# Kernel tuning notes

Hardware: AMD Instinct MI355X
Metric: run time of the kernel (lower is better)

Reference implementation:

```python
import jax, jax.numpy as jnp
import numpy as np

B, S, DM, H = 4, 2048, 512, 8
HD = DM // H


def setup_inputs() -> dict:
    key = jax.random.key(0)
    ks = jax.random.split(key, 12)
    x = jax.random.normal(ks[0], (B, S, DM), dtype=jnp.float32)
    # causal lower-triangular mask [B, S, S]
    mask = jnp.broadcast_to(jnp.tril(jnp.ones((S, S), dtype=jnp.int32)), (B, S, S))
    # sorted irregular day offsets (trading-day-like), in days
    days_offset = jnp.sort(
        jax.random.uniform(ks[1], (B, S), dtype=jnp.float32) * 3000.0, axis=-1
    )
    scale = 1.0 / np.sqrt(DM)
    Wq = jax.random.normal(ks[2], (DM, DM), dtype=jnp.float32) * scale
    bq = jnp.zeros((DM,), dtype=jnp.float32)
    Wk = jax.random.normal(ks[3], (DM, DM), dtype=jnp.float32) * scale
    bk = jnp.zeros((DM,), dtype=jnp.float32)
    Wv = jax.random.normal(ks[4], (DM, DM), dtype=jnp.float32) * scale
    bv = jnp.zeros((DM,), dtype=jnp.float32)
    Wo = jax.random.normal(ks[5], (DM, DM), dtype=jnp.float32) * scale
    bo = jnp.zeros((DM,), dtype=jnp.float32)
    decay_rate = jnp.float32(0.1)
    return {
        "x": x, "mask": mask, "days_offset": days_offset,
        "Wq": Wq, "bq": bq, "Wk": Wk, "bk": bk,
        "Wv": Wv, "bv": bv, "Wo": Wo, "bo": bo,
        "decay_rate": decay_rate,
    }


def reference(x, mask, days_offset, Wq, bq, Wk, bk, Wv, bv, Wo, bo, decay_rate):
    b, s, _ = x.shape
    # projections (torch Linear: x @ W.T + b), split heads -> [b, h, s, hd]
    def proj(W, bias):
        return (x @ W.T + bias).reshape(b, s, H, HD).transpose(0, 2, 1, 3)
    q, k, v = proj(Wq, bq), proj(Wk, bk), proj(Wv, bv)
    scores = jnp.einsum("bhqd,bhkd->bhqk", q, k) / jnp.sqrt(jnp.float32(HD))
    # temporal decay: exp(-rate * |t_i - t_j|), broadcast over heads
    dist = jnp.abs(days_offset[:, :, None] - days_offset[:, None, :])  # [b,s,s]
    decay = jnp.exp(-decay_rate * dist)
    scores = scores * decay[:, None, :, :]
    scores = jnp.where(mask[:, None, :, :] == 0, -jnp.inf, scores)
    attn = jax.nn.softmax(scores, axis=-1)  # dropout p=0 (eval)
    out = jnp.einsum("bhqk,bhkd->bhqd", attn, v)
    out = out.transpose(0, 2, 1, 3).reshape(b, s, DM)
    return out @ Wo.T + bo
```

## Files before the change

### kernel.cpp

```cpp
#include <hip/hip_runtime.h>
#include <hip/hip_fp16.h>


#define S_LEN 2048
#define DMODEL 512
#define NH 8
#define HD 64

typedef _Float16 half8 __attribute__((ext_vector_type(8)));
typedef _Float16 half4 __attribute__((ext_vector_type(4)));
typedef float floatx4 __attribute__((ext_vector_type(4)));

__device__ __forceinline__ void gload16(const _Float16* g, _Float16* l) {
    __builtin_amdgcn_global_load_lds(
        (const __attribute__((address_space(1))) void*)g,
        (__attribute__((address_space(3))) void*)l, 16, 0, 0);
}

__global__ __launch_bounds__(256) void cast_f32_f16(
    const float* __restrict__ x,
    const float* __restrict__ Wq, const float* __restrict__ Wk,
    const float* __restrict__ Wv, const float* __restrict__ Wo,
    _Float16* __restrict__ xh, _Float16* __restrict__ Wh)
{
    int i = blockIdx.x * 256 + threadIdx.x;
    const float* src; _Float16* dst; int off;
    if (i < 1048576) { src = x; dst = xh; off = i; }
    else {
        int j = i - 1048576;
        int w = j >> 16;
        int within = j & 65535;
        src = (w == 0) ? Wq : (w == 1) ? Wk : (w == 2) ? Wv : Wo;
        dst = Wh + w * (DMODEL * DMODEL);
        off = within;
    }
    float4 v = ((const float4*)src)[off];
    half4 h;
    h.x = (_Float16)v.x; h.y = (_Float16)v.y; h.z = (_Float16)v.z; h.w = (_Float16)v.w;
    *(half4*)(dst + (size_t)off * 4) = h;
}

template <int MODE>
__global__ __launch_bounds__(256) void gemm_k(
    const _Float16* __restrict__ A, const _Float16* __restrict__ Wbase,
    const float* __restrict__ b0, const float* __restrict__ b1,
    const float* __restrict__ b2,
    _Float16* __restrict__ outh, float* __restrict__ outf)
{
    __shared__ _Float16 As[128 * 64];
    __shared__ _Float16 Ws[128 * 64];
    const int t = threadIdx.x;
    const int bm = blockIdx.x, bn = blockIdx.y, z = blockIdx.z;
    const _Float16* Wp = Wbase + (MODE == 0 ? z * (DMODEL * DMODEL) : 0);
    const float* bias = (MODE == 0) ? (z == 0 ? b0 : (z == 1 ? b1 : b2)) : b0;
    const int w = t >> 6, lane = t & 63, l15 = lane & 15, quad = lane >> 4;
    const int wrow = (w >> 1) * 64, wcol = (w & 1) * 64;
    const int lrow = lane >> 3;
    const int sw = (lane & 7) ^ lrow;

    floatx4 acc[4][4] = {};
    for (int kb = 0; kb < 8; ++kb) {
        __syncthreads();
        #pragma unroll
        for (int i = 0; i < 4; ++i) {
            int row0 = w * 32 + i * 8;
            gload16(A  + (size_t)(bm * 128 + row0 + lrow) * DMODEL + kb * 64 + sw * 8, &As[row0 * 64]);
            gload16(Wp + (size_t)(bn * 128 + row0 + lrow) * DMODEL + kb * 64 + sw * 8, &Ws[row0 * 64]);
        }
        __syncthreads();
        #pragma unroll
        for (int kk = 0; kk < 2; ++kk) {
            half8 af[4], bf[4];
            #pragma unroll
            for (int mt = 0; mt < 4; ++mt)
                af[mt] = *(const half8*)(&As[(wrow + mt * 16 + l15) * 64 + (((quad + 4 * kk) ^ (l15 & 7)) * 8)]);
            #pragma unroll
            for (int nt = 0; nt < 4; ++nt)
                bf[nt] = *(const half8*)(&Ws[(wcol + nt * 16 + l15) * 64 + (((quad + 4 * kk) ^ (l15 & 7)) * 8)]);
            #pragma unroll
            for (int mt = 0; mt < 4; ++mt)
                #pragma unroll
                for (int nt = 0; nt < 4; ++nt)
                    acc[mt][nt] = __builtin_amdgcn_mfma_f32_16x16x32_f16(af[mt], bf[nt], acc[mt][nt], 0, 0, 0);
        }
    }
    #pragma unroll
    for (int mt = 0; mt < 4; ++mt)
        #pragma unroll
        for (int nt = 0; nt < 4; ++nt) {
            int n = bn * 128 + wcol + nt * 16 + l15;
            float bvv = bias[n];
            if (MODE == 0 && z == 2) {
                int m0 = bm * 128 + wrow + mt * 16 + quad * 4;
                int b = m0 >> 11, s0 = m0 & 2047;
                int hh = n >> 6, hd = n & 63;
                half4 hv;
                #pragma unroll
                for (int r = 0; r < 4; ++r) hv[r] = (_Float16)(acc[mt][nt][r] + bvv);
                *(half4*)(outh + (size_t)2 * (8192 * 512) +
                          ((size_t)(b * NH + hh) * HD + hd) * S_LEN + s0) = hv;
            } else {
                #pragma unroll
                for (int r = 0; r < 4; ++r) {
                    int m = bm * 128 + wrow + mt * 16 + quad * 4 + r;
                    float val = acc[mt][nt][r] + bvv;
                    if (MODE == 0) {
                        int b = m >> 11, s = m & 2047;
                        int hh = n >> 6, hd = n & 63;
                        outh[(size_t)z * (8192 * 512) +
                             ((size_t)(b * NH + hh) * S_LEN + s) * HD + hd] = (_Float16)val;
                    } else {
                        outf[(size_t)m * DMODEL + n] = val;
                    }
                }
            }
        }
}

__global__ __launch_bounds__(256, 1) void attn_k(
    const _Float16* __restrict__ Qh, const _Float16* __restrict__ Kh,
    const _Float16* __restrict__ Vt, const float* __restrict__ days,
    const float* __restrict__ rate_p, _Float16* __restrict__ Ah)
{
    __shared__ _Float16 Ks[2][64 * 64];
    __shared__ _Float16 Vs[2][64 * 64];
    __shared__ float    eks[2][64];
    __shared__ _Float16 Ps[4][2][16 * 64];

    const int pr = blockIdx.x, h = blockIdx.y, b = blockIdx.z;
    const int t = threadIdx.x, w = t >> 6, lane = t & 63, l15 = lane & 15, quad = lane >> 4;
    const float rate = rate_p[0];
    const size_t bhoff = (size_t)(b * NH + h) * (size_t)(S_LEN * HD);
    const _Float16* Qb = Qh + bhoff;
    const _Float16* Kb = Kh + bhoff;
    const _Float16* Vb = Vt + bhoff;
    const float* daysb = days + b * S_LEN;
    const int lrow = lane >> 3, sw = (lane & 7) ^ lrow;
    const int e7 = l15 & 7;

    auto stage = [&](int kt, int buf) {
        #pragma unroll
        for (int i = 0; i < 2; ++i) {
            int grp = w * 2 + i;
            int row = grp * 8 + lrow;
            gload16(Kb + (size_t)(kt * 64 + row) * HD + sw * 8, &Ks[buf][grp * 512]);
            gload16(Vb + (size_t)row * S_LEN + kt * 64 + sw * 8, &Vs[buf][grp * 512]);
        }
        if (w == 0) {
            float tk0 = daysb[kt * 64];
            float d = daysb[kt * 64 + lane];
            eks[buf][lane] = __expf(fminf(rate * (d - tk0), 80.f));
        }
    };

    auto phase = [&](int qb) {
        const int q0 = qb * 128 + w * 32;
        const int KT = 2 * qb + 1;
        half8 qf[2][2];
        float tq[2]; int qg[2];
        #pragma unroll
        for (int qs = 0; qs < 2; ++qs) {
            qg[qs] = q0 + qs * 16 + l15;
            tq[qs] = daysb[qg[qs]];
            #pragma unroll
            for (int kk = 0; kk < 2; ++kk)
                qf[qs][kk] = *(const half8*)(Qb + (size_t)qg[qs] * HD + kk * 32 + quad * 8);
        }
        floatx4 oacc[2][4] = {};
        float lacc[2] = {0.f, 0.f};

        stage(0, 0);
        for (int kt = 0; kt <= KT; ++kt) {
            __syncthreads();
            if (kt < KT) stage(kt + 1, (kt + 1) & 1);
            const int buf = kt & 1;
            const float tk0 = daysb[kt * 64];
            half8 kf[4][2];
            #pragma unroll
            for (int c = 0; c < 4; ++c)
                #pragma unroll
                for (int kk = 0; kk < 2; ++kk)
                    kf[c][kk] = *(const half8*)(&Ks[buf][(c * 16 + l15) * 64 + (((quad + 4 * kk) ^ e7) * 8)]);
            floatx4 sc[2][4];
            #pragma unroll
            for (int qs = 0; qs < 2; ++qs)
                #pragma unroll
                for (int c = 0; c < 4; ++c) {
                    floatx4 z4 = {};
                    z4 = __builtin_amdgcn_mfma_f32_16x16x32_f16(kf[c][0], qf[qs][0], z4, 0, 0, 0);
                    sc[qs][c] = __builtin_amdgcn_mfma_f32_16x16x32_f16(kf[c][1], qf[qs][1], z4, 0, 0, 0);
                }
            half8 vf[4][2];
            #pragma unroll
            for (int s = 0; s < 4; ++s)
                #pragma unroll
                for (int kk = 0; kk < 2; ++kk)
                    vf[s][kk] = *(const half8*)(&Vs[buf][(s * 16 + l15) * 64 + (((quad + 4 * kk) ^ e7) * 8)]);
            floatx4 ekv[4];
            #pragma unroll
            for (int c = 0; c < 4; ++c)
                ekv[c] = *(const floatx4*)(&eks[buf][c * 16 + quad * 4]);
            float eq[2];
            #pragma unroll
            for (int qs = 0; qs < 2; ++qs)
                eq[qs] = 0.125f * __expf(-rate * (tq[qs] - tk0));
            const bool nm = (kt >= 2 * qb);
            #pragma unroll
            for (int qs = 0; qs < 2; ++qs) {
                #pragma unroll
                for (int c = 0; c < 4; ++c) {
                    float pv[4];
                    #pragma unroll
                    for (int r = 0; r < 4; ++r) {
                        float sv = sc[qs][c][r] * (eq[qs] * ekv[c][r]);
                        float p = __expf(sv - 2.0f);
                        if (nm && (kt * 64 + c * 16 + quad * 4 + r) > qg[qs]) p = 0.f;
                        lacc[qs] += p;
                        pv[r] = p;
                    }
                    half4 hv;
                    hv.x = (_Float16)pv[0]; hv.y = (_Float16)pv[1];
                    hv.z = (_Float16)pv[2]; hv.w = (_Float16)pv[3];
                    *(half4*)(&Ps[w][qs][l15 * 64 + (((2 * c + (quad >> 1)) ^ e7) * 8) + (quad & 1) * 4]) = hv;
                }
            }
            #pragma unroll
            for (int qs = 0; qs < 2; ++qs) {
                half8 pf0 = *(const half8*)(&Ps[w][qs][l15 * 64 + ((quad ^ e7) * 8)]);
                half8 pf1 = *(const half8*)(&Ps[w][qs][l15 * 64 + (((4 + quad) ^ e7) * 8)]);
                #pragma unroll
                for (int s = 0; s < 4; ++s) {
                    oacc[qs][s] = __builtin_amdgcn_mfma_f32_16x16x32_f16(vf[s][0], pf0, oacc[qs][s], 0, 0, 0);
                    oacc[qs][s] = __builtin_amdgcn_mfma_f32_16x16x32_f16(vf[s][1], pf1, oacc[qs][s], 0, 0, 0);
                }
            }
        }

        #pragma unroll
        for (int qs = 0; qs < 2; ++qs) {
            float l = lacc[qs];
            l += __shfl_xor(l, 16);
            l += __shfl_xor(l, 32);
            float linv = 1.0f / l;
            #pragma unroll
            for (int s = 0; s < 4; ++s) {
                half4 hv;
                #pragma unroll
                for (int r = 0; r < 4; ++r) hv[r] = (_Float16)(oacc[qs][s][r] * linv);
                *(half4*)(Ah + ((size_t)(b * S_LEN) + qg[qs]) * DMODEL + h * HD + s * 16 + quad * 4) = hv;
            }
        }
    };

    phase(pr);
    phase(15 - pr);
}

extern "C" void kernel_launch(void* const* d_in, const int* in_sizes, int n_in,
                              void* d_out, int out_size, void* d_ws, size_t ws_size,
                              hipStream_t stream)
{
    const float* x    = (const float*)d_in[0];
    const float* days = (const float*)d_in[2];
    const float* Wq   = (const float*)d_in[3];
    const float* bq   = (const float*)d_in[4];
    const float* Wk   = (const float*)d_in[5];
    const float* bk   = (const float*)d_in[6];
    const float* Wv   = (const float*)d_in[7];
    const float* bv   = (const float*)d_in[8];
    const float* Wo   = (const float*)d_in[9];
    const float* bo   = (const float*)d_in[10];
    const float* rate = (const float*)d_in[11];
    float* out = (float*)d_out;

    _Float16* xh = (_Float16*)d_ws;
    _Float16* Wh = xh + 4194304;
    _Float16* Qh = Wh + 1048576;
    _Float16* Kh = Qh + 4194304;
    _Float16* Vh = Kh + 4194304;
    _Float16* Ah = Vh + 4194304;

    cast_f32_f16<<<5120, 256, 0, stream>>>(x, Wq, Wk, Wv, Wo, xh, Wh);

    dim3 g0(64, 4, 3);
    gemm_k<0><<<g0, 256, 0, stream>>>(xh, Wh, bq, bk, bv, Qh, nullptr);

    dim3 ga(8, NH, 4);
    attn_k<<<ga, 256, 0, stream>>>(Qh, Kh, Vh, days, rate, Ah);

    dim3 g1(64, 4, 1);
    gemm_k<1><<<g1, 256, 0, stream>>>(Ah, Wh + 3 * (DMODEL * DMODEL), bo, bo, bo, nullptr, out);
}
```

Before: 223.4 us.

## Halve attention query tile, double grid, and stage GEMM epilogue through LDS

The attention kernel now gives each wave 16 query rows instead of 32 and pairs 64-row query blocks j and 31-j. This doubles the grid to 512 blocks and lets two blocks share a CU (launch bounds 256,2), which should improve occupancy and balance the causal work. It also prefetches the first K/V tile of the second phase while the first phase finishes. The GEMM epilogue for Q/K and the output projection now goes through an LDS buffer so global stores are 16-byte vectors instead of scattered scalar writes. The cost is less K/V reuse per staged tile and extra LDS traffic in the epilogue.

Result: faster. 206.9 us (-7.4%).

```diff
diff --git a/kernel.cpp b/kernel.cpp
--- a/kernel.cpp
+++ b/kernel.cpp
@@ -49,6 +49,7 @@
 {
     __shared__ _Float16 As[128 * 64];
     __shared__ _Float16 Ws[128 * 64];
+    __shared__ char epbuf[MODE == 0 ? (4 * 16 * 72 * 2) : (4 * 16 * 68 * 4)];
     const int t = threadIdx.x;
     const int bm = blockIdx.x, bn = blockIdx.y, z = blockIdx.z;
     const _Float16* Wp = Wbase + (MODE == 0 ? z * (DMODEL * DMODEL) : 0);
@@ -84,13 +85,14 @@
                     acc[mt][nt] = __builtin_amdgcn_mfma_f32_16x16x32_f16(af[mt], bf[nt], acc[mt][nt], 0, 0, 0);
         }
     }
-    #pragma unroll
-    for (int mt = 0; mt < 4; ++mt)
-        #pragma unroll
-        for (int nt = 0; nt < 4; ++nt) {
-            int n = bn * 128 + wcol + nt * 16 + l15;
-            float bvv = bias[n];
-            if (MODE == 0 && z == 2) {
+
+    if (MODE == 0 && z == 2) {
+        #pragma unroll
+        for (int mt = 0; mt < 4; ++mt)
+            #pragma unroll
+            for (int nt = 0; nt < 4; ++nt) {
+                int n = bn * 128 + wcol + nt * 16 + l15;
+                float bvv = bias[n];
                 int m0 = bm * 128 + wrow + mt * 16 + quad * 4;
                 int b = m0 >> 11, s0 = m0 & 2047;
                 int hh = n >> 6, hd = n & 63;
@@ -99,25 +101,55 @@
                 for (int r = 0; r < 4; ++r) hv[r] = (_Float16)(acc[mt][nt][r] + bvv);
                 *(half4*)(outh + (size_t)2 * (8192 * 512) +
                           ((size_t)(b * NH + hh) * HD + hd) * S_LEN + s0) = hv;
-            } else {
-                #pragma unroll
-                for (int r = 0; r < 4; ++r) {
-                    int m = bm * 128 + wrow + mt * 16 + quad * 4 + r;
-                    float val = acc[mt][nt][r] + bvv;
-                    if (MODE == 0) {
-                        int b = m >> 11, s = m & 2047;
-                        int hh = n >> 6, hd = n & 63;
-                        outh[(size_t)z * (8192 * 512) +
-                             ((size_t)(b * NH + hh) * S_LEN + s) * HD + hd] = (_Float16)val;
-                    } else {
-                        outf[(size_t)m * DMODEL + n] = val;
-                    }
+            }
+    } else {
+        float bv4[4];
+        #pragma unroll
+        for (int nt = 0; nt < 4; ++nt) bv4[nt] = bias[bn * 128 + wcol + nt * 16 + l15];
+        const int rr = lane >> 3, cc = (lane & 7) ^ rr;
+        if (MODE == 0) {
+            _Float16* Ep = (_Float16*)epbuf + w * (16 * 72);
+            const int hq = (bn * 128 + wcol) >> 6;
+            #pragma unroll
+            for (int mt = 0; mt < 4; ++mt) {
+                #pragma unroll
+                for (int nt = 0; nt < 4; ++nt)
+                    #pragma unroll
+                    for (int r = 0; r < 4; ++r)
+                        Ep[(quad * 4 + r) * 72 + nt * 16 + l15] = (_Float16)(acc[mt][nt][r] + bv4[nt]);
+                #pragma unroll
+                for (int i2 = 0; i2 < 2; ++i2) {
+                    int row = i2 * 8 + rr;
+                    half8 v = *(const half8*)(&Ep[row * 72 + cc * 8]);
+                    int m = bm * 128 + wrow + mt * 16 + row;
+                    int bb = m >> 11, ss = m & 2047;
+                    *(half8*)(outh + (size_t)z * (8192 * 512) +
+                              ((size_t)(bb * NH + hq) * S_LEN + ss) * HD + cc * 8) = v;
                 }
             }
-        }
-}
-
-__global__ __launch_bounds__(256, 1) void attn_k(
+        } else {
+            float* Epf = (float*)epbuf + w * (16 * 68);
+            #pragma unroll
+            for (int mt = 0; mt < 4; ++mt) {
+                #pragma unroll
+                for (int nt = 0; nt < 4; ++nt)
+                    #pragma unroll
+                    for (int r = 0; r < 4; ++r)
+                        Epf[(quad * 4 + r) * 68 + nt * 16 + l15] = acc[mt][nt][r] + bv4[nt];
+                #pragma unroll
+                for (int i2 = 0; i2 < 4; ++i2) {
+                    int row = (i2 & 1) * 8 + rr;
+                    int ch = cc + (i2 >> 1) * 8;
+                    float4 v = *(const float4*)(&Epf[row * 68 + ch * 4]);
+                    int m = bm * 128 + wrow + mt * 16 + row;
+                    *(float4*)(outf + (size_t)m * DMODEL + bn * 128 + wcol + ch * 4) = v;
+                }
+            }
+        }
+    }
+}
+
+__global__ __launch_bounds__(256, 2) void attn_k(
     const _Float16* __restrict__ Qh, const _Float16* __restrict__ Kh,
     const _Float16* __restrict__ Vt, const float* __restrict__ days,
     const float* __restrict__ rate_p, _Float16* __restrict__ Ah)
@@ -125,7 +157,7 @@
     __shared__ _Float16 Ks[2][64 * 64];
     __shared__ _Float16 Vs[2][64 * 64];
     __shared__ float    eks[2][64];
-    __shared__ _Float16 Ps[4][2][16 * 64];
+    __shared__ _Float16 Ps[4][16 * 64];
 
     const int pr = blockIdx.x, h = blockIdx.y, b = blockIdx.z;
     const int t = threadIdx.x, w = t >> 6, lane = t & 63, l15 = lane & 15, quad = lane >> 4;
@@ -153,107 +185,88 @@
         }
     };
 
-    auto phase = [&](int qb) {
-        const int q0 = qb * 128 + w * 32;
-        const int KT = 2 * qb + 1;
-        half8 qf[2][2];
-        float tq[2]; int qg[2];
-        #pragma unroll
-        for (int qs = 0; qs < 2; ++qs) {
-            qg[qs] = q0 + qs * 16 + l15;
-            tq[qs] = daysb[qg[qs]];
-            #pragma unroll
-            for (int kk = 0; kk < 2; ++kk)
-                qf[qs][kk] = *(const half8*)(Qb + (size_t)qg[qs] * HD + kk * 32 + quad * 8);
-        }
-        floatx4 oacc[2][4] = {};
-        float lacc[2] = {0.f, 0.f};
-
-        stage(0, 0);
-        for (int kt = 0; kt <= KT; ++kt) {
+    auto run_phase = [&](int j, int par0, int nextj) -> int {
+        const int qg = j * 64 + w * 16 + l15;
+        half8 qf0 = *(const half8*)(Qb + (size_t)qg * HD + quad * 8);
+        half8 qf1 = *(const half8*)(Qb + (size_t)qg * HD + 32 + quad * 8);
+        const float tq = daysb[qg];
+        floatx4 oacc[4] = {};
+        float lacc = 0.f;
+
+        for (int kt = 0; kt <= j; ++kt) {
+            const int par = (par0 + kt) & 1;
             __syncthreads();
-            if (kt < KT) stage(kt + 1, (kt + 1) & 1);
-            const int buf = kt & 1;
+            if (kt < j) stage(kt + 1, par ^ 1);
+            else if (nextj >= 0) stage(0, par ^ 1);
             const float tk0 = daysb[kt * 64];
             half8 kf[4][2];
             #pragma unroll
             for (int c = 0; c < 4; ++c)
                 #pragma unroll
                 for (int kk = 0; kk < 2; ++kk)
-                    kf[c][kk] = *(const half8*)(&Ks[buf][(c * 16 + l15) * 64 + (((quad + 4 * kk) ^ e7) * 8)]);
-            floatx4 sc[2][4];
-            #pragma unroll
-            for (int qs = 0; qs < 2; ++qs)
-                #pragma unroll
-                for (int c = 0; c < 4; ++c) {
-                    floatx4 z4 = {};
-                    z4 = __builtin_amdgcn_mfma_f32_16x16x32_f16(kf[c][0], qf[qs][0], z4, 0, 0, 0);
-                    sc[qs][c] = __builtin_amdgcn_mfma_f32_16x16x32_f16(kf[c][1], qf[qs][1], z4, 0, 0, 0);
+                    kf[c][kk] = *(const half8*)(&Ks[par][(c * 16 + l15) * 64 + (((quad + 4 * kk) ^ e7) * 8)]);
+            floatx4 sc[4];
+            #pragma unroll
+            for (int c = 0; c < 4; ++c) {
+                floatx4 z4 = {};
+                z4 = __builtin_amdgcn_mfma_f32_16x16x32_f16(kf[c][0], qf0, z4, 0, 0, 0);
+                sc[c] = __builtin_amdgcn_mfma_f32_16x16x32_f16(kf[c][1], qf1, z4, 0, 0, 0);
+            }
+            half8 vf[4][2];
+            #pragma unroll
+            for (int s4 = 0; s4 < 4; ++s4)
+                #pragma unroll
+                for (int kk = 0; kk < 2; ++kk)
+                    vf[s4][kk] = *(const half8*)(&Vs[par][(s4 * 16 + l15) * 64 + (((quad + 4 * kk) ^ e7) * 8)]);
+            floatx4 ekv[4];
+            #pragma unroll
+            for (int c = 0; c < 4; ++c)
+                ekv[c] = *(const floatx4*)(&eks[par][c * 16 + quad * 4]);
+            const float eq = 0.125f * __expf(-rate * (tq - tk0));
+            const bool dg = (kt == j);
+            #pragma unroll
+            for (int c = 0; c < 4; ++c) {
+                float pvv[4];
+                #pragma unroll
+                for (int r = 0; r < 4; ++r) {
+                    float sv = sc[c][r] * (eq * ekv[c][r]);
+                    float p = __expf(sv - 2.0f);
+                    if (dg && (kt * 64 + c * 16 + quad * 4 + r) > qg) p = 0.f;
+                    lacc += p;
+                    pvv[r] = p;
                 }
-            half8 vf[4][2];
-            #pragma unroll
-            for (int s = 0; s < 4; ++s)
-                #pragma unroll
-                for (int kk = 0; kk < 2; ++kk)
-                    vf[s][kk] = *(const half8*)(&Vs[buf][(s * 16 + l15) * 64 + (((quad + 4 * kk) ^ e7) * 8)]);
-            floatx4 ekv[4];
-            #pragma unroll
-            for (int c = 0; c < 4; ++c)
-                ekv[c] = *(const floatx4*)(&eks[buf][c * 16 + quad * 4]);
-            float eq[2];
-            #pragma unroll
-            for (int qs = 0; qs < 2; ++qs)
-                eq[qs] = 0.125f * __expf(-rate * (tq[qs] - tk0));
-            const bool nm = (kt >= 2 * qb);
-            #pragma unroll
-            for (int qs = 0; qs < 2; ++qs) {
-                #pragma unroll
-                for (int c = 0; c < 4; ++c) {
-                    float pv[4];
-                    #pragma unroll
-                    for (int r = 0; r < 4; ++r) {
-                        float sv = sc[qs][c][r] * (eq[qs] * ekv[c][r]);
-                        float p = __expf(sv - 2.0f);
-                        if (nm && (kt * 64 + c * 16 + quad * 4 + r) > qg[qs]) p = 0.f;
-                        lacc[qs] += p;
-                        pv[r] = p;
-                    }
-                    half4 hv;
-                    hv.x = (_Float16)pv[0]; hv.y = (_Float16)pv[1];
-                    hv.z = (_Float16)pv[2]; hv.w = (_Float16)pv[3];
-                    *(half4*)(&Ps[w][qs][l15 * 64 + (((2 * c + (quad >> 1)) ^ e7) * 8) + (quad & 1) * 4]) = hv;
-                }
-            }
-            #pragma unroll
-            for (int qs = 0; qs < 2; ++qs) {
-                half8 pf0 = *(const half8*)(&Ps[w][qs][l15 * 64 + ((quad ^ e7) * 8)]);
-                half8 pf1 = *(const half8*)(&Ps[w][qs][l15 * 64 + (((4 + quad) ^ e7) * 8)]);
-                #pragma unroll
-                for (int s = 0; s < 4; ++s) {
-                    oacc[qs][s] = __builtin_amdgcn_mfma_f32_16x16x32_f16(vf[s][0], pf0, oacc[qs][s], 0, 0, 0);
-                    oacc[qs][s] = __builtin_amdgcn_mfma_f32_16x16x32_f16(vf[s][1], pf1, oacc[qs][s], 0, 0, 0);
-                }
-            }
-        }
-
-        #pragma unroll
-        for (int qs = 0; qs < 2; ++qs) {
-            float l = lacc[qs];
-            l += __shfl_xor(l, 16);
-            l += __shfl_xor(l, 32);
-            float linv = 1.0f / l;
-            #pragma unroll
-            for (int s = 0; s < 4; ++s) {
                 half4 hv;
-                #pragma unroll
-                for (int r = 0; r < 4; ++r) hv[r] = (_Float16)(oacc[qs][s][r] * linv);
-                *(half4*)(Ah + ((size_t)(b * S_LEN) + qg[qs]) * DMODEL + h * HD + s * 16 + quad * 4) = hv;
-            }
-        }
+                hv.x = (_Float16)pvv[0]; hv.y = (_Float16)pvv[1];
+                hv.z = (_Float16)pvv[2]; hv.w = (_Float16)pvv[3];
+                *(half4*)(&Ps[w][l15 * 64 + (((2 * c + (quad >> 1)) ^ e7) * 8) + (quad & 1) * 4]) = hv;
+            }
+            half8 pf0 = *(const half8*)(&Ps[w][l15 * 64 + ((quad ^ e7) * 8)]);
+            half8 pf1 = *(const half8*)(&Ps[w][l15 * 64 + (((4 + quad) ^ e7) * 8)]);
+            #pragma unroll
+            for (int s4 = 0; s4 < 4; ++s4) {
+                oacc[s4] = __builtin_amdgcn_mfma_f32_16x16x32_f16(vf[s4][0], pf0, oacc[s4], 0, 0, 0);
+                oacc[s4] = __builtin_amdgcn_mfma_f32_16x16x32_f16(vf[s4][1], pf1, oacc[s4], 0, 0, 0);
+            }
+        }
+
+        float l = lacc;
+        l += __shfl_xor(l, 16);
+        l += __shfl_xor(l, 32);
+        float linv = 1.0f / l;
+        #pragma unroll
+        for (int s4 = 0; s4 < 4; ++s4) {
+            half4 hv;
+            #pragma unroll
+            for (int r = 0; r < 4; ++r) hv[r] = (_Float16)(oacc[s4][r] * linv);
+            *(half4*)(Ah + ((size_t)(b * S_LEN) + qg) * DMODEL + h * HD + s4 * 16 + quad * 4) = hv;
+        }
+        return (par0 + j + 1) & 1;
     };
 
-    phase(pr);
-    phase(15 - pr);
+    const int j0 = pr, j1 = 31 - pr;
+    stage(0, 0);
+    int p1 = run_phase(j0, 0, j1);
+    run_phase(j1, p1, -1);
 }
 
 extern "C" void kernel_launch(void* const* d_in, const int* in_sizes, int n_in,
@@ -285,7 +298,7 @@
     dim3 g0(64, 4, 3);
     gemm_k<0><<<g0, 256, 0, stream>>>(xh, Wh, bq, bk, bv, Qh, nullptr);
 
-    dim3 ga(8, NH, 4);
+    dim3 ga(16, NH, 4);
     attn_k<<<ga, 256, 0, stream>>>(Qh, Kh, Vh, days, rate, Ah);
 
     dim3 g1(64, 4, 1);
```
